# Kernel optimization log

Measured on AMD Instinct MI355X. Metric: run time of the kernel, lower is better.

The kernel has to match this reference:

```python
import jax, jax.numpy as jnp
import numpy as np

BATCH, INPUTDIM, OUTDIM, GRIDSIZE = 4096, 256, 256, 64


def setup_inputs() -> dict:
    key = jax.random.key(0)
    k1, k2 = jax.random.split(key)
    x = jax.random.normal(k1, (BATCH, INPUTDIM), dtype=jnp.float32)
    # xavier_uniform over (2, outdim, inputdim, gridsize): fan_in = inputdim*gridsize, fan_out = outdim*gridsize
    fan_in = INPUTDIM * GRIDSIZE
    fan_out = OUTDIM * GRIDSIZE
    limit = float(np.sqrt(6.0 / (fan_in + fan_out)))
    fouriercoeffs = jax.random.uniform(
        k2, (2, OUTDIM, INPUTDIM, GRIDSIZE), dtype=jnp.float32,
        minval=-limit, maxval=limit)
    bias = jnp.zeros((1, OUTDIM), dtype=jnp.float32)
    return {"x": x, "fouriercoeffs": fouriercoeffs, "bias": bias}


def reference(x, fouriercoeffs, bias):
    # x: [B, inputdim]; fouriercoeffs: [2, outdim, inputdim, gridsize]; bias: [1, outdim]
    # gridsize_param is clamp/round'ed to an int in torch -> static = initial_gridsize here.
    G = fouriercoeffs.shape[-1]
    k = jnp.arange(1, G + 1, dtype=x.dtype)        # [G] frequencies 1..G
    xk = x[:, :, None] * k                          # [B, inputdim, G]
    c = jnp.cos(xk)                                 # [B, inputdim, G]
    s = jnp.sin(xk)                                 # [B, inputdim, G]
    # Fused contraction over (inputdim, gridsize) -- avoids the naive
    # [B, outdim, inputdim, gridsize] broadcast tensor of the torch code.
    y = (jnp.einsum('big,oig->bo', c, fouriercoeffs[0])
         + jnp.einsum('big,oig->bo', s, fouriercoeffs[1])
         + bias)                                    # [B, outdim]
    return y
```

## Files before the change

kernel.cpp:

```cpp
#include <hip/hip_runtime.h>
#include <hip/hip_bf16.h>


typedef __attribute__((ext_vector_type(8))) short short8;
typedef __attribute__((ext_vector_type(16))) float f32x16;

#define SPLITK 16
#define ICHUNK (256 / SPLITK)

#define INV2PI 0.15915494309189535f

__device__ __forceinline__ unsigned short f2bf(float f) {
    unsigned u = __builtin_bit_cast(unsigned, f);
    u += 0x7fffu + ((u >> 16) & 1u);
    return (unsigned short)(u >> 16);
}
#if __has_builtin(__builtin_amdgcn_cvt_pk_bf16_f32)
typedef __attribute__((ext_vector_type(2))) __bf16 bf16x2_t;
__device__ __forceinline__ unsigned pkbf16(float a, float b) {
    bf16x2_t v = __builtin_amdgcn_cvt_pk_bf16_f32(a, b);
    return __builtin_bit_cast(unsigned, v);
}
#else
__device__ __forceinline__ unsigned pkbf16(float a, float b) {
    unsigned ua = __builtin_bit_cast(unsigned, a) + 0x8000u;
    unsigned ub = __builtin_bit_cast(unsigned, b) + 0x8000u;
    return __builtin_amdgcn_perm(ub, ua, 0x07060302u);
}
#endif

__device__ __forceinline__ void dbl2(float c, float s, float& co, float& so) {
    float t = c + c;
    co = __builtin_fmaf(t, c, -1.f);
    so = t * s;
}
__device__ __forceinline__ void rot2(float c, float s, float cr, float sr,
                                     float& co, float& so) {
    float t = s * sr;
    co = __builtin_fmaf(c, cr, -t);
    float u = s * cr;
    so = __builtin_fmaf(c, sr, u);
}

__device__ __forceinline__ short8 chain8(float m1, float fm1, float f0) {
    unsigned r[4];
    float vp = fm1, v = f0;
    #pragma unroll
    for (int h = 0; h < 4; ++h) {
        float v1 = __builtin_fmaf(m1, v, -vp);
        r[h] = pkbf16(v, v1);
        float v2 = __builtin_fmaf(m1, v1, -v);
        vp = v1; v = v2;
    }
    uint4 u; u.x = r[0]; u.y = r[1]; u.z = r[2]; u.w = r[3];
    return __builtin_bit_cast(short8, u);
}

__device__ __forceinline__ void async_load16(const void* g, void* l) {
    __builtin_amdgcn_global_load_lds(
        (const __attribute__((address_space(1))) unsigned int*)g,
        (__attribute__((address_space(3))) unsigned int*)l,
        16, 0, 0);
}

__global__ __launch_bounds__(512) void prep_kernel(
    const float* __restrict__ fc, unsigned short* __restrict__ ws2)
{
    __shared__ unsigned pk[512][36];
    const int i = blockIdx.x;
    const int t = threadIdx.x;
    const int rr  = t >> 4;
    const int l16 = t & 15;

    #pragma unroll
    for (int p = 0; p < 16; ++p) {
        int r = p * 32 + rr;
        const float4* src =
            (const float4*)(fc + ((size_t)r * 256 + i) * 64) + l16;
        float4 v = *src;
        pk[r][l16 * 2]     = pkbf16(v.x, v.y);
        pk[r][l16 * 2 + 1] = pkbf16(v.z, v.w);
    }
    __syncthreads();

    #pragma unroll
    for (int gg = 0; gg < 8; ++gg) {
        int gi = gg * 512 + t;
        int sog = gi >> 6, ll = gi & 63;
        int ks = sog >> 3, cb = sog & 7;
        int o  = cb * 32 + (ll & 31);
        int kb = ks * 16 + (ll >> 5) * 8;
        int tt = kb >> 6, g0 = kb & 63;
        int r = tt * 256 + o;
        int c = g0 >> 1;
        uint4 v;
        v.x = pk[r][c]; v.y = pk[r][c + 1];
        v.z = pk[r][c + 2]; v.w = pk[r][c + 3];
        ((uint4*)ws2)[(size_t)i * 4096 + gi] = v;
    }
}

__global__ __launch_bounds__(256) void bias_init(
    const float* __restrict__ bias, float* __restrict__ out)
{
    int idx4 = blockIdx.x * 256 + threadIdx.x;
    ((float4*)out)[idx4] = ((const float4*)bias)[idx4 & 63];
}

__global__ __launch_bounds__(256) void reduce_kernel(
    const unsigned short* __restrict__ pws, const float* __restrict__ bias,
    float* __restrict__ out)
{
    int idx4 = blockIdx.x * 256 + threadIdx.x;
    float4 r = ((const float4*)bias)[idx4 & 63];
    #pragma unroll
    for (int z = 0; z < SPLITK; ++z) {
        ushort4 v = ((const ushort4*)pws)[(size_t)z * 262144 + idx4];
        r.x += __builtin_bit_cast(float, (unsigned)v.x << 16);
        r.y += __builtin_bit_cast(float, (unsigned)v.y << 16);
        r.z += __builtin_bit_cast(float, (unsigned)v.z << 16);
        r.w += __builtin_bit_cast(float, (unsigned)v.w << 16);
    }
    ((float4*)out)[idx4] = r;
}

template <bool USE_WS, bool PARTIAL>
__global__ __launch_bounds__(512, 2) void fkan_gemm(
    const float* __restrict__ x, const float* __restrict__ fc,
    const unsigned short* __restrict__ bws, float* __restrict__ out,
    unsigned short* __restrict__ pws)
{
    __shared__ uint4 Bimg[2][4096];
    __shared__ float xs[ICHUNK][256];

    const int t  = threadIdx.x;
    const int l  = t & 63;
    const int w  = t >> 6;
    const int rg = w >> 1;
    const int cg = w & 1;
    const int m32 = l & 31;
    const int h  = l >> 5;

    const int bid = blockIdx.x;
    const int z   = bid & 15;
    const int bx  = bid >> 4;
    const int rowBase = bx * 256;
    const int iBase   = z * ICHUNK;

    f32x16 acc[2][4];
    #pragma unroll
    for (int a = 0; a < 2; ++a)
        #pragma unroll
        for (int b = 0; b < 4; ++b) acc[a][b] = (f32x16)0.0f;

    auto stageB = [&](int p, int i) {
        if (USE_WS) {
            const uint4* base = (const uint4*)bws + (size_t)i * 4096;
            #pragma unroll
            for (int cc = 0; cc < 8; ++cc) {
                int c = cc * 8 + w;
                async_load16(base + (size_t)c * 64 + l, (void*)(&Bimg[p][c * 64]));
            }
        } else {
            #pragma unroll
            for (int gg = 0; gg < 8; ++gg) {
                int gi  = gg * 512 + t;
                int sog = gi >> 6, ll = gi & 63;
                int ks = sog >> 3, cb = sog & 7;
                int o  = cb * 32 + (ll & 31);
                int kb = ks * 16 + (ll >> 5) * 8;
                int tt = kb >> 6, g0 = kb & 63;
                const float4* p4 = (const float4*)(fc +
                    ((((size_t)tt * 256 + o) * 256 + i) * 64 + g0));
                float4 a = p4[0], b = p4[1];
                uint4 v;
                v.x = pkbf16(a.x, a.y); v.y = pkbf16(a.z, a.w);
                v.z = pkbf16(b.x, b.y); v.w = pkbf16(b.z, b.w);
                Bimg[p][gi] = v;
            }
        }
    };

    stageB(0, iBase);
    {
        const int row = t >> 1;
        const int hf  = t & 1;
        const float4* px =
            (const float4*)(x + (size_t)(rowBase + row) * 256 + iBase) + hf * 2;
        float4 v0 = px[0], v1 = px[1];
        int c0 = hf * 8;
        xs[c0 + 0][row] = v0.x; xs[c0 + 1][row] = v0.y;
        xs[c0 + 2][row] = v0.z; xs[c0 + 3][row] = v0.w;
        xs[c0 + 4][row] = v1.x; xs[c0 + 5][row] = v1.y;
        xs[c0 + 6][row] = v1.z; xs[c0 + 7][row] = v1.w;
    }
    __syncthreads();

    #pragma unroll 1
    for (int ii = 0; ii < ICHUNK; ++ii) {
        const int p = ii & 1;

        if (ii + 1 < ICHUNK) stageB(p ^ 1, iBase + ii + 1);

        short8 aF[2][8];
        #pragma unroll
        for (int rf = 0; rf < 2; ++rf) {
            float xv = xs[ii][rg * 64 + rf * 32 + m32];
            float rev = xv * INV2PI;
            float s1 = __builtin_amdgcn_sinf(rev);
            float c1 = __builtin_amdgcn_cosf(rev);
            const float m1 = c1 + c1;
            float c2, s2, c4, s4, c8, s8, c16, s16;
            dbl2(c1, s1, c2, s2);
            dbl2(c2, s2, c4, s4);
            dbl2(c4, s4, c8, s8);
            dbl2(c8, s8, c16, s16);
            float cB = h ? c8 : 1.f;
            float sB = h ? s8 : 0.f;
            #pragma unroll
            for (int k = 0; k < 4; ++k) {
                float cB1, sB1;
                rot2(cB, sB, c1, s1, cB1, sB1);
                aF[rf][k]     = chain8(m1, cB, cB1);
                aF[rf][4 + k] = chain8(m1, sB, sB1);
                if (k < 3) {
                    float cN, sN;
                    rot2(cB, sB, c16, s16, cN, sN);
                    cB = cN; sB = sN;
                }
            }
        }

        #pragma unroll
        for (int ks = 0; ks < 8; ++ks) {
            short8 bF[4];
            #pragma unroll
            for (int cf = 0; cf < 4; ++cf)
                bF[cf] = __builtin_bit_cast(short8,
                    Bimg[p][(ks * 8 + cg * 4 + cf) * 64 + l]);
            #pragma unroll
            for (int rf = 0; rf < 2; ++rf)
                #pragma unroll
                for (int cf = 0; cf < 4; ++cf)
                    acc[rf][cf] = __builtin_amdgcn_mfma_f32_32x32x16_bf16(
                        aF[rf][ks], bF[cf], acc[rf][cf], 0, 0, 0);
        }

        __syncthreads();
    }

    const int r0 = rowBase + rg * 64 + h * 4;
    const int c0 = cg * 128 + m32;
    if (PARTIAL) {
        unsigned short* dst = pws + (size_t)z * (4096u * 256u);
        #pragma unroll
        for (int rf = 0; rf < 2; ++rf)
            #pragma unroll
            for (int cf = 0; cf < 4; ++cf)
                #pragma unroll
                for (int e = 0; e < 16; ++e) {
                    int rl = (e & 3) + 8 * (e >> 2);
                    dst[(size_t)(r0 + rf * 32 + rl) * 256 + (c0 + cf * 32)] =
                        f2bf(acc[rf][cf][e]);
                }
    } else {
        #pragma unroll
        for (int rf = 0; rf < 2; ++rf)
            #pragma unroll
            for (int cf = 0; cf < 4; ++cf)
                #pragma unroll
                for (int e = 0; e < 16; ++e) {
                    int rl = (e & 3) + 8 * (e >> 2);
                    atomicAdd(out + (size_t)(r0 + rf * 32 + rl) * 256 + (c0 + cf * 32),
                              acc[rf][cf][e]);
                }
    }
}

extern "C" void kernel_launch(void* const* d_in, const int* in_sizes, int n_in,
                              void* d_out, int out_size, void* d_ws, size_t ws_size,
                              hipStream_t stream) {
    const float* x    = (const float*)d_in[0];
    const float* fc   = (const float*)d_in[1];
    const float* bias = (const float*)d_in[2];
    float* out = (float*)d_out;
    unsigned short* bws = (unsigned short*)d_ws;

    const size_t wsCoeff = (size_t)256 * 4096 * 16;
    const size_t wsFull  = wsCoeff + (size_t)SPLITK * 4096 * 256 * 2;
    unsigned short* pws = (unsigned short*)((char*)d_ws + wsCoeff);

    if (ws_size >= wsFull) {
        hipLaunchKernelGGL(prep_kernel, dim3(256), dim3(512), 0, stream, fc, bws);
        hipLaunchKernelGGL((fkan_gemm<true, true>), dim3(256), dim3(512), 0, stream,
                           x, fc, bws, out, pws);
        hipLaunchKernelGGL(reduce_kernel, dim3(1024), dim3(256), 0, stream,
                           pws, bias, out);
    } else if (ws_size >= wsCoeff) {
        hipLaunchKernelGGL(bias_init, dim3(1024), dim3(256), 0, stream, bias, out);
        hipLaunchKernelGGL(prep_kernel, dim3(256), dim3(512), 0, stream, fc, bws);
        hipLaunchKernelGGL((fkan_gemm<true, false>), dim3(256), dim3(512), 0, stream,
                           x, fc, bws, out, pws);
    } else {
        hipLaunchKernelGGL(bias_init, dim3(1024), dim3(256), 0, stream, bias, out);
        hipLaunchKernelGGL((fkan_gemm<false, false>), dim3(256), dim3(512), 0, stream,
                           x, fc, bws, out, pws);
    }
}
```

Baseline: 157.1 us.

## Halve GEMM block tile and single-buffer B to fit two blocks per CU

The main GEMM kernel goes from 512 threads and 256 rows to 256 threads and 128 rows per block, with the grid doubled to 512 blocks. The double-buffered B tile in LDS becomes a single buffer, so each block needs about half the shared memory and more blocks can be resident per CU. The loop now runs MFMA, syncs, then issues the next B stage and computes the next sin/cos fragments, then syncs again. In-block overlap of B loading with MFMA is traded for overlap across co-resident blocks, and each B chunk is now fetched by twice as many blocks.

New measurement: 157.9 us. About the same (+0.5%).

```diff
diff --git a/kernel.cpp b/kernel.cpp
--- a/kernel.cpp
+++ b/kernel.cpp
@@ -125,13 +125,13 @@
 }
 
 template <bool USE_WS, bool PARTIAL>
-__global__ __launch_bounds__(512, 2) void fkan_gemm(
+__global__ __launch_bounds__(256, 2) void fkan_gemm(
     const float* __restrict__ x, const float* __restrict__ fc,
     const unsigned short* __restrict__ bws, float* __restrict__ out,
     unsigned short* __restrict__ pws)
 {
-    __shared__ uint4 Bimg[2][4096];
-    __shared__ float xs[ICHUNK][256];
+    __shared__ uint4 Bimg[4096];
+    __shared__ float xs[ICHUNK][128];
 
     const int t  = threadIdx.x;
     const int l  = t & 63;
@@ -144,7 +144,7 @@
     const int bid = blockIdx.x;
     const int z   = bid & 15;
     const int bx  = bid >> 4;
-    const int rowBase = bx * 256;
+    const int rowBase = bx * 128;
     const int iBase   = z * ICHUNK;
 
     f32x16 acc[2][4];
@@ -153,18 +153,20 @@
         #pragma unroll
         for (int b = 0; b < 4; ++b) acc[a][b] = (f32x16)0.0f;
 
-    auto stageB = [&](int p, int i) {
+    short8 aF[2][8];
+
+    auto stageB = [&](int i) {
         if (USE_WS) {
             const uint4* base = (const uint4*)bws + (size_t)i * 4096;
             #pragma unroll
-            for (int cc = 0; cc < 8; ++cc) {
-                int c = cc * 8 + w;
-                async_load16(base + (size_t)c * 64 + l, (void*)(&Bimg[p][c * 64]));
+            for (int cc = 0; cc < 16; ++cc) {
+                int c = cc * 4 + w;
+                async_load16(base + (size_t)c * 64 + l, (void*)(&Bimg[c * 64]));
             }
         } else {
             #pragma unroll
-            for (int gg = 0; gg < 8; ++gg) {
-                int gi  = gg * 512 + t;
+            for (int gg = 0; gg < 16; ++gg) {
+                int gi  = gg * 256 + t;
                 int sog = gi >> 6, ll = gi & 63;
                 int ks = sog >> 3, cb = sog & 7;
                 int o  = cb * 32 + (ll & 31);
@@ -176,33 +178,12 @@
                 uint4 v;
                 v.x = pkbf16(a.x, a.y); v.y = pkbf16(a.z, a.w);
                 v.z = pkbf16(b.x, b.y); v.w = pkbf16(b.z, b.w);
-                Bimg[p][gi] = v;
+                Bimg[gi] = v;
             }
         }
     };
 
-    stageB(0, iBase);
-    {
-        const int row = t >> 1;
-        const int hf  = t & 1;
-        const float4* px =
-            (const float4*)(x + (size_t)(rowBase + row) * 256 + iBase) + hf * 2;
-        float4 v0 = px[0], v1 = px[1];
-        int c0 = hf * 8;
-        xs[c0 + 0][row] = v0.x; xs[c0 + 1][row] = v0.y;
-        xs[c0 + 2][row] = v0.z; xs[c0 + 3][row] = v0.w;
-        xs[c0 + 4][row] = v1.x; xs[c0 + 5][row] = v1.y;
-        xs[c0 + 6][row] = v1.z; xs[c0 + 7][row] = v1.w;
-    }
-    __syncthreads();
-
-    #pragma unroll 1
-    for (int ii = 0; ii < ICHUNK; ++ii) {
-        const int p = ii & 1;
-
-        if (ii + 1 < ICHUNK) stageB(p ^ 1, iBase + ii + 1);
-
-        short8 aF[2][8];
+    auto synth = [&](int ii) {
         #pragma unroll
         for (int rf = 0; rf < 2; ++rf) {
             float xv = xs[ii][rg * 64 + rf * 32 + m32];
@@ -230,23 +211,57 @@
                 }
             }
         }
-
+    };
+
+    auto mfmaFull = [&]() {
         #pragma unroll
         for (int ks = 0; ks < 8; ++ks) {
             short8 bF[4];
             #pragma unroll
             for (int cf = 0; cf < 4; ++cf)
                 bF[cf] = __builtin_bit_cast(short8,
-                    Bimg[p][(ks * 8 + cg * 4 + cf) * 64 + l]);
-            #pragma unroll
-            for (int rf = 0; rf < 2; ++rf)
-                #pragma unroll
-                for (int cf = 0; cf < 4; ++cf)
-                    acc[rf][cf] = __builtin_amdgcn_mfma_f32_32x32x16_bf16(
-                        aF[rf][ks], bF[cf], acc[rf][cf], 0, 0, 0);
+                    Bimg[(ks * 8 + cg * 4 + cf) * 64 + l]);
+            #pragma unroll
+            for (int cf = 0; cf < 4; ++cf) {
+                acc[0][cf] = __builtin_amdgcn_mfma_f32_32x32x16_bf16(
+                    aF[0][ks], bF[cf], acc[0][cf], 0, 0, 0);
+                acc[1][cf] = __builtin_amdgcn_mfma_f32_32x32x16_bf16(
+                    aF[1][ks], bF[cf], acc[1][cf], 0, 0, 0);
+            }
         }
-
+    };
+
+    auto loadXs = [&]() {
+        const int row = t >> 1;
+        const int hf  = t & 1;
+        const float4* px =
+            (const float4*)(x + (size_t)(rowBase + row) * 256 + iBase) + hf * 2;
+        float4 v0 = px[0], v1 = px[1];
+        int c0 = hf * 8;
+        xs[c0 + 0][row] = v0.x; xs[c0 + 1][row] = v0.y;
+        xs[c0 + 2][row] = v0.z; xs[c0 + 3][row] = v0.w;
+        xs[c0 + 4][row] = v1.x; xs[c0 + 5][row] = v1.y;
+        xs[c0 + 6][row] = v1.z; xs[c0 + 7][row] = v1.w;
+    };
+
+    stageB(iBase);
+    loadXs();
+    __syncthreads();
+    asm volatile("" ::: "memory");
+    synth(0);
+
+    #pragma unroll 1
+    for (int ii = 0; ii < ICHUNK; ++ii) {
+        mfmaFull();
         __syncthreads();
+        asm volatile("" ::: "memory");
+
+        if (ii + 1 < ICHUNK) {
+            stageB(iBase + ii + 1);
+            synth(ii + 1);
+            __syncthreads();
+            asm volatile("" ::: "memory");
+        }
     }
 
     const int r0 = rowBase + rg * 64 + h * 4;
@@ -292,18 +307,18 @@
 
     if (ws_size >= wsFull) {
         hipLaunchKernelGGL(prep_kernel, dim3(256), dim3(512), 0, stream, fc, bws);
-        hipLaunchKernelGGL((fkan_gemm<true, true>), dim3(256), dim3(512), 0, stream,
+        hipLaunchKernelGGL((fkan_gemm<true, true>), dim3(512), dim3(256), 0, stream,
                            x, fc, bws, out, pws);
         hipLaunchKernelGGL(reduce_kernel, dim3(1024), dim3(256), 0, stream,
                            pws, bias, out);
     } else if (ws_size >= wsCoeff) {
         hipLaunchKernelGGL(bias_init, dim3(1024), dim3(256), 0, stream, bias, out);
         hipLaunchKernelGGL(prep_kernel, dim3(256), dim3(512), 0, stream, fc, bws);
-        hipLaunchKernelGGL((fkan_gemm<true, false>), dim3(256), dim3(512), 0, stream,
+        hipLaunchKernelGGL((fkan_gemm<true, false>), dim3(512), dim3(256), 0, stream,
                            x, fc, bws, out, pws);
     } else {
         hipLaunchKernelGGL(bias_init, dim3(1024), dim3(256), 0, stream, bias, out);
-        hipLaunchKernelGGL((fkan_gemm<false, false>), dim3(256), dim3(512), 0, stream,
+        hipLaunchKernelGGL((fkan_gemm<false, false>), dim3(512), dim3(256), 0, stream,
                            x, fc, bws, out, pws);
     }
 }
```
